# Optimization experiments

Measured on AMD Instinct MI355X. Metric: run time of the kernel, lower is better.

The kernel has to match this reference:

```python
import jax, jax.numpy as jnp
import numpy as np

N_ROUTINGS = 3
NEG_SLOPE = 0.01  # torch leaky_relu default


def l2norm(x, eps=1e-12):
    # torch.nn.functional.normalize along dim=1
    n = jnp.sqrt(jnp.sum(x * x, axis=1, keepdims=True))
    return x / jnp.maximum(n, eps)


def seg_softmax(w, seg, n):
    # numerically-stable softmax over edges grouped by node id `seg`
    m = jax.ops.segment_max(w, seg, num_segments=n)
    e = jnp.exp(w - m[seg])
    s = jax.ops.segment_sum(e, seg, num_segments=n)
    return e / (s[seg] + 1e-16)


def setup_inputs() -> dict:
    key = jax.random.key(0)
    ks = jax.random.split(key, 8)
    NU, NI, D, F, E, B = 100000, 50000, 64, 2048, 2000000, 4096
    return {
        "Gum": jax.random.normal(ks[0], (NU, D), dtype=jnp.float32),
        "feat": jax.random.normal(ks[1], (NI, F), dtype=jnp.float32),
        "proj_w": jax.random.normal(ks[2], (F, D), dtype=jnp.float32) * 0.02,
        "proj_b": jax.random.normal(ks[3], (D,), dtype=jnp.float32) * 0.02,
        "rows": jax.random.randint(ks[4], (E,), 0, NU, dtype=jnp.int32),
        "cols": jax.random.randint(ks[5], (E,), 0, NI, dtype=jnp.int32),
        "user": jax.random.randint(ks[6], (B,), 0, NU, dtype=jnp.int32),
        "pos": jax.random.randint(ks[7], (B,), 0, NI, dtype=jnp.int32),
    }


def reference(Gum, feat, proj_w, proj_b, rows, cols, user, pos):
    NU = Gum.shape[0]
    NI = feat.shape[0]
    # user multimodal preference embeddings, normalized
    gum = l2norm(Gum)
    # item multimodal content: normalize features, project, leaky_relu, normalize
    gim = l2norm(jax.nn.leaky_relu(l2norm(feat) @ proj_w + proj_b, NEG_SLOPE))
    cols_attr = gim[cols]  # [E, D] gathered once (as in original)
    # routing iterations: refine user preference via attention over item neighbors
    for _ in range(N_ROUTINGS):
        rows_attr = gum[rows]                                   # [E, D] gather
        w = jax.nn.leaky_relu(jnp.sum(rows_attr * cols_attr, -1), NEG_SLOPE)
        alpha = seg_softmax(w, rows, NU)                        # per-user softmax
        upd = jax.ops.segment_sum(alpha[:, None] * cols_attr, rows, num_segments=NU)
        gum = l2norm(gum + upd)
    # final refining layer on the full (symmetric) interaction graph
    rows_attr = gum[rows]
    w = jax.nn.leaky_relu(jnp.sum(rows_attr * cols_attr, -1), NEG_SLOPE)
    a_u = seg_softmax(w, rows, NU)
    a_i = seg_softmax(w, cols, NI)
    hat_u = jax.ops.segment_sum(a_u[:, None] * cols_attr, rows, num_segments=NU)
    hat_i = jax.ops.segment_sum(a_i[:, None] * rows_attr, cols, num_segments=NI)
    gu = gum + hat_u   # all_x_m += all_x_hat_m (user part)
    gi = gim + hat_i   # (item part)
    # model.forward: elementwise dot of gathered user/item embeddings
    xui = jnp.sum(gu[user] * gi[pos], axis=1)  # [B]
    return xui
```

## Files before the change

kernel.cpp:

```cpp
#include <hip/hip_runtime.h>
#include <math.h>

#define RCAP 16

__device__ __forceinline__ int wsumi(int v) {
#pragma unroll
    for (int o = 32; o > 0; o >>= 1) v += __shfl_xor(v, o, 64);
    return v;
}
__device__ __forceinline__ float grp16_sum(float v) {
    v += __shfl_xor(v, 1, 64);
    v += __shfl_xor(v, 2, 64);
    v += __shfl_xor(v, 4, 64);
    v += __shfl_xor(v, 8, 64);
    return v;
}
__device__ __forceinline__ float xgrp_sum(float v) {
    v += __shfl_xor(v, 16, 64);
    v += __shfl_xor(v, 32, 64);
    return v;
}
__device__ __forceinline__ float4 xgrp_sum4(float4 a) {
    a.x = xgrp_sum(a.x); a.y = xgrp_sum(a.y);
    a.z = xgrp_sum(a.z); a.w = xgrp_sum(a.w);
    return a;
}

__global__ void k_gim(const float* __restrict__ feat, const float* __restrict__ W,
                      const float* __restrict__ bias, float* __restrict__ gim,
                      int NI, int F) {
    __shared__ float As[64][17];
    __shared__ float Bs[16][64];
    __shared__ float rn[64];
    const int tid = threadIdx.x;
    const int r0 = blockIdx.x * 64;
    const int tr = tid >> 4, tc = tid & 15;
    const int lrow = tid >> 2, lk = (tid & 3) * 4;
    float acc[4][4];
#pragma unroll
    for (int i = 0; i < 4; ++i)
#pragma unroll
        for (int j = 0; j < 4; ++j) acc[i][j] = 0.f;
    float ssq = 0.f;
    const bool rowok = (r0 + lrow) < NI;

    for (int kb = 0; kb < F; kb += 16) {
        float4 av = make_float4(0.f, 0.f, 0.f, 0.f);
        if (rowok) av = *(const float4*)(feat + (size_t)(r0 + lrow) * F + kb + lk);
        As[lrow][lk + 0] = av.x; As[lrow][lk + 1] = av.y;
        As[lrow][lk + 2] = av.z; As[lrow][lk + 3] = av.w;
        ssq += av.x * av.x + av.y * av.y + av.z * av.z + av.w * av.w;
        float4 bv = *(const float4*)(W + (size_t)(kb + (tid >> 4)) * 64 + (tid & 15) * 4);
        *(float4*)&Bs[tid >> 4][(tid & 15) * 4] = bv;
        __syncthreads();
#pragma unroll
        for (int kk = 0; kk < 16; ++kk) {
            float a[4], b[4];
#pragma unroll
            for (int i = 0; i < 4; ++i) a[i] = As[tr * 4 + i][kk];
#pragma unroll
            for (int j = 0; j < 4; ++j) b[j] = Bs[kk][tc * 4 + j];
#pragma unroll
            for (int i = 0; i < 4; ++i)
#pragma unroll
                for (int j = 0; j < 4; ++j) acc[i][j] += a[i] * b[j];
        }
        __syncthreads();
    }
    ssq += __shfl_xor(ssq, 1, 64);
    ssq += __shfl_xor(ssq, 2, 64);
    if ((tid & 3) == 0) rn[lrow] = ssq;
    __syncthreads();

    float bc[4];
#pragma unroll
    for (int j = 0; j < 4; ++j) bc[j] = bias[tc * 4 + j];
#pragma unroll
    for (int i = 0; i < 4; ++i) {
        int r = tr * 4 + i;
        float inv = 1.0f / fmaxf(sqrtf(rn[r]), 1e-12f);
        float v[4], rs = 0.f;
#pragma unroll
        for (int j = 0; j < 4; ++j) {
            float x = acc[i][j] * inv + bc[j];
            x = x > 0.f ? x : 0.01f * x;
            v[j] = x; rs += x * x;
        }
        rs += __shfl_xor(rs, 1, 64); rs += __shfl_xor(rs, 2, 64);
        rs += __shfl_xor(rs, 4, 64); rs += __shfl_xor(rs, 8, 64);
        float sc = 1.0f / fmaxf(sqrtf(rs), 1e-12f);
        int gr = r0 + r;
        if (gr < NI) {
            float4 o = make_float4(v[0] * sc, v[1] * sc, v[2] * sc, v[3] * sc);
            *(float4*)(gim + (size_t)gr * 64 + tc * 4) = o;
        }
    }
}

__global__ void k_hist(const int* __restrict__ rows, const int* __restrict__ cols, int E,
                       int* __restrict__ cu, int* __restrict__ ci,
                       int* __restrict__ ranku, int* __restrict__ ranki) {
    for (int e = blockIdx.x * blockDim.x + threadIdx.x; e < E; e += gridDim.x * blockDim.x) {
        ranku[e] = atomicAdd(&cu[rows[e]], 1);
        ranki[e] = atomicAdd(&ci[cols[e]], 1);
    }
}

__global__ void k_bsum(const int* __restrict__ cnt, int n, int* __restrict__ bsum) {
    int i = blockIdx.x * 256 + threadIdx.x;
    int v = (i < n) ? cnt[i] : 0;
    v = wsumi(v);
    __shared__ int sm[4];
    if ((threadIdx.x & 63) == 0) sm[threadIdx.x >> 6] = v;
    __syncthreads();
    if (threadIdx.x == 0) bsum[blockIdx.x] = sm[0] + sm[1] + sm[2] + sm[3];
}

__global__ void k_bscan(const int* __restrict__ bsum, int nb, int* __restrict__ bscan) {
    __shared__ int sd[512];
    int tid = threadIdx.x;
    int v = (tid < nb) ? bsum[tid] : 0;
    sd[tid] = v;
    __syncthreads();
    for (int off = 1; off < 512; off <<= 1) {
        int t = (tid >= off) ? sd[tid - off] : 0;
        __syncthreads();
        sd[tid] += t;
        __syncthreads();
    }
    if (tid < nb) bscan[tid] = sd[tid] - v;
}

__global__ void k_scan2(const int* __restrict__ cnt, int n, const int* __restrict__ bscan,
                        int* __restrict__ ptr) {
    __shared__ int sd[256];
    int tid = threadIdx.x;
    int i = blockIdx.x * 256 + tid;
    int v = (i < n) ? cnt[i] : 0;
    sd[tid] = v;
    __syncthreads();
    for (int off = 1; off < 256; off <<= 1) {
        int t = (tid >= off) ? sd[tid - off] : 0;
        __syncthreads();
        sd[tid] += t;
        __syncthreads();
    }
    if (i < n) ptr[i + 1] = sd[tid] + bscan[blockIdx.x];
    if (blockIdx.x == 0 && tid == 0) ptr[0] = 0;
}

__global__ void k_scatter(const int* __restrict__ rows, const int* __restrict__ cols, int E,
                          const int* __restrict__ ranku, const int* __restrict__ ranki,
                          const int* __restrict__ rptr, const int* __restrict__ cptr,
                          int2* __restrict__ csr, int* __restrict__ csc_r) {
    for (int e = blockIdx.x * blockDim.x + threadIdx.x; e < E; e += gridDim.x * blockDim.x) {
        int r = rows[e], c = cols[e];
        int pu = rptr[r] + ranku[e];
        int pi = cptr[c] + ranki[e];
        csr[pu] = make_int2(c, pi);
        csc_r[pi] = r;
    }
}

__global__ void __launch_bounds__(256) k_route(
        const float* __restrict__ Gum, const float* __restrict__ gim,
        const int* __restrict__ rptr, const int2* __restrict__ csr,
        float* __restrict__ gum_out, float* __restrict__ gu,
        float* __restrict__ expw_csc, int NU) {
    __shared__ float tile[4 * RCAP * 64];
    int wid = (blockIdx.x * blockDim.x + threadIdx.x) >> 6;
    int lane = threadIdx.x & 63;
    if (wid >= NU) return;
    const int q = lane >> 4, r = lane & 15;
    float* my = tile + (threadIdx.x >> 6) * (RCAP * 64);
    const size_t ubase = (size_t)wid * 64 + 4 * r;

    float4 gl = *(const float4*)(Gum + ubase);
    float s2 = grp16_sum(gl.x * gl.x + gl.y * gl.y + gl.z * gl.z + gl.w * gl.w);
    float inv = 1.0f / fmaxf(sqrtf(s2), 1e-12f);
    gl.x *= inv; gl.y *= inv; gl.z *= inv; gl.w *= inv;

    const int st = rptr[wid], en = rptr[wid + 1];
    const int enc = min(en, st + RCAP);

    {
        float s = 0.f;
        float4 acc = make_float4(0.f, 0.f, 0.f, 0.f);
        for (int j0 = st; j0 < en; j0 += 4) {
            int j = j0 + q;
            bool valid = j < en;
            int c = valid ? csr[j].x : 0;
            float4 gv = *(const float4*)(gim + (size_t)c * 64 + 4 * r);
            if (j < enc) *(float4*)(my + (j - st) * 64 + 4 * r) = gv;
            float d = grp16_sum(gl.x * gv.x + gl.y * gv.y + gl.z * gv.z + gl.w * gv.w);
            float w = d > 0.f ? d : 0.01f * d;
            float ew = valid ? __expf(w) : 0.f;
            s += ew;
            acc.x += ew * gv.x; acc.y += ew * gv.y;
            acc.z += ew * gv.z; acc.w += ew * gv.w;
        }
        s = xgrp_sum(s);
        acc = xgrp_sum4(acc);
        float invs = 1.0f / (s + 1e-16f);
        gl.x += acc.x * invs; gl.y += acc.y * invs;
        gl.z += acc.z * invs; gl.w += acc.w * invs;
        s2 = grp16_sum(gl.x * gl.x + gl.y * gl.y + gl.z * gl.z + gl.w * gl.w);
        inv = 1.0f / fmaxf(sqrtf(s2), 1e-12f);
        gl.x *= inv; gl.y *= inv; gl.z *= inv; gl.w *= inv;
    }

    for (int it = 0; it < 2; ++it) {
        float s = 0.f;
        float4 acc = make_float4(0.f, 0.f, 0.f, 0.f);
        for (int j0 = st; j0 < en; j0 += 4) {
            int j = j0 + q;
            bool valid = j < en;
            float4 gv;
            if (j < enc) {
                gv = *(const float4*)(my + (j - st) * 64 + 4 * r);
            } else {
                int c = valid ? csr[j].x : 0;
                gv = *(const float4*)(gim + (size_t)c * 64 + 4 * r);
            }
            float d = grp16_sum(gl.x * gv.x + gl.y * gv.y + gl.z * gv.z + gl.w * gv.w);
            float w = d > 0.f ? d : 0.01f * d;
            float ew = valid ? __expf(w) : 0.f;
            s += ew;
            acc.x += ew * gv.x; acc.y += ew * gv.y;
            acc.z += ew * gv.z; acc.w += ew * gv.w;
        }
        s = xgrp_sum(s);
        acc = xgrp_sum4(acc);
        float invs = 1.0f / (s + 1e-16f);
        gl.x += acc.x * invs; gl.y += acc.y * invs;
        gl.z += acc.z * invs; gl.w += acc.w * invs;
        s2 = grp16_sum(gl.x * gl.x + gl.y * gl.y + gl.z * gl.z + gl.w * gl.w);
        inv = 1.0f / fmaxf(sqrtf(s2), 1e-12f);
        gl.x *= inv; gl.y *= inv; gl.z *= inv; gl.w *= inv;
    }
    if (q == 0) *(float4*)(gum_out + ubase) = gl;

    float s = 0.f;
    float4 acc = make_float4(0.f, 0.f, 0.f, 0.f);
    for (int j0 = st; j0 < en; j0 += 4) {
        int j = j0 + q;
        bool valid = j < en;
        float4 gv;
        if (j < enc) {
            gv = *(const float4*)(my + (j - st) * 64 + 4 * r);
        } else {
            int c = valid ? csr[j].x : 0;
            gv = *(const float4*)(gim + (size_t)c * 64 + 4 * r);
        }
        float d = grp16_sum(gl.x * gv.x + gl.y * gv.y + gl.z * gv.z + gl.w * gv.w);
        float w = d > 0.f ? d : 0.01f * d;
        float ew = valid ? __expf(w) : 0.f;
        if (valid && r == 0) expw_csc[csr[j].y] = ew;
        s += ew;
        acc.x += ew * gv.x; acc.y += ew * gv.y;
        acc.z += ew * gv.z; acc.w += ew * gv.w;
    }
    s = xgrp_sum(s);
    acc = xgrp_sum4(acc);
    float invs = 1.0f / (s + 1e-16f);
    if (q == 0) {
        float4 o = make_float4(gl.x + acc.x * invs, gl.y + acc.y * invs,
                               gl.z + acc.z * invs, gl.w + acc.w * invs);
        *(float4*)(gu + ubase) = o;
    }
}

__global__ void k_item(const float* __restrict__ gum, const float* __restrict__ gim,
                       const int* __restrict__ cptr, const int* __restrict__ csc_r,
                       const float* __restrict__ expw_csc,
                       float* __restrict__ gi, int NI) {
    int wid = (blockIdx.x * blockDim.x + threadIdx.x) >> 6;
    int lane = threadIdx.x & 63;
    if (wid >= NI) return;
    const int q = lane >> 4, r = lane & 15;
    const int st = cptr[wid], en = cptr[wid + 1];
    float s = 0.f;
    float4 acc = make_float4(0.f, 0.f, 0.f, 0.f);
    for (int j0 = st; j0 < en; j0 += 4) {
        int j = j0 + q;
        bool valid = j < en;
        int rr = valid ? csc_r[j] : 0;
        float ew = valid ? expw_csc[j] : 0.f;
        float4 gv = *(const float4*)(gum + (size_t)rr * 64 + 4 * r);
        s += ew;
        acc.x += ew * gv.x; acc.y += ew * gv.y;
        acc.z += ew * gv.z; acc.w += ew * gv.w;
    }
    s = xgrp_sum(s);
    acc = xgrp_sum4(acc);
    float invs = 1.0f / (s + 1e-16f);
    if (q == 0) {
        const size_t ib = (size_t)wid * 64 + 4 * r;
        float4 gm = *(const float4*)(gim + ib);
        float4 o = make_float4(gm.x + acc.x * invs, gm.y + acc.y * invs,
                               gm.z + acc.z * invs, gm.w + acc.w * invs);
        *(float4*)(gi + ib) = o;
    }
}

__global__ void k_out(const float* __restrict__ gu, const float* __restrict__ gi,
                      const int* __restrict__ user, const int* __restrict__ pos,
                      float* __restrict__ out, int B) {
    int wid = (blockIdx.x * blockDim.x + threadIdx.x) >> 6;
    int lane = threadIdx.x & 63;
    if (wid >= B) return;
    float v = gu[(size_t)user[wid] * 64 + lane] * gi[(size_t)pos[wid] * 64 + lane];
#pragma unroll
    for (int o = 32; o > 0; o >>= 1) v += __shfl_xor(v, o, 64);
    if (lane == 0) out[wid] = v;
}

extern "C" void kernel_launch(void* const* d_in, const int* in_sizes, int n_in,
                              void* d_out, int out_size, void* d_ws, size_t ws_size,
                              hipStream_t stream) {
    const float* Gum  = (const float*)d_in[0];
    const float* feat = (const float*)d_in[1];
    const float* W    = (const float*)d_in[2];
    const float* bias = (const float*)d_in[3];
    const int* rows   = (const int*)d_in[4];
    const int* cols   = (const int*)d_in[5];
    const int* user   = (const int*)d_in[6];
    const int* pos    = (const int*)d_in[7];
    float* out = (float*)d_out;

    const int D  = in_sizes[3];
    const int NU = in_sizes[0] / D;
    const int F  = in_sizes[2] / D;
    const int NI = in_sizes[1] / F;
    const int E  = in_sizes[4];
    const int B  = in_sizes[6];

    char* p = (char*)d_ws;
    auto alloc = [&](size_t bytes) -> void* {
        void* r = (void*)p;
        p += (bytes + 255) / 256 * 256;
        return r;
    };
    float* gum     = (float*)alloc((size_t)NU * 64 * 4);
    float* gim     = (float*)alloc((size_t)NI * 64 * 4);
    float* gu      = (float*)alloc((size_t)NU * 64 * 4);
    float* gi      = (float*)alloc((size_t)NI * 64 * 4);
    float* expw    = (float*)alloc((size_t)E * 4);
    int* rptr      = (int*)alloc((size_t)(NU + 1) * 4);
    int* cptr      = (int*)alloc((size_t)(NI + 1) * 4);
    int* cu        = (int*)alloc((size_t)NU * 4);
    int* ci        = (int*)alloc((size_t)NI * 4);
    int* ranku     = (int*)alloc((size_t)E * 4);
    int* ranki     = (int*)alloc((size_t)E * 4);
    int2* csr      = (int2*)alloc((size_t)E * 8);
    int* csc_r     = (int*)alloc((size_t)E * 4);
    int* bsumU     = (int*)alloc(1024 * 4);
    int* bscanU    = (int*)alloc(1024 * 4);
    int* bsumI     = (int*)alloc(1024 * 4);
    int* bscanI    = (int*)alloc(1024 * 4);

    const int gU = (NU + 255) / 256;
    const int gI = (NI + 255) / 256;

    hipMemsetAsync(cu, 0, (size_t)NU * 4, stream);
    hipMemsetAsync(ci, 0, (size_t)NI * 4, stream);
    k_hist<<<2048, 256, 0, stream>>>(rows, cols, E, cu, ci, ranku, ranki);

    k_bsum<<<gU, 256, 0, stream>>>(cu, NU, bsumU);
    k_bscan<<<1, 512, 0, stream>>>(bsumU, gU, bscanU);
    k_scan2<<<gU, 256, 0, stream>>>(cu, NU, bscanU, rptr);

    k_bsum<<<gI, 256, 0, stream>>>(ci, NI, bsumI);
    k_bscan<<<1, 512, 0, stream>>>(bsumI, gI, bscanI);
    k_scan2<<<gI, 256, 0, stream>>>(ci, NI, bscanI, cptr);

    k_scatter<<<2048, 256, 0, stream>>>(rows, cols, E, ranku, ranki, rptr, cptr, csr, csc_r);

    k_gim<<<(NI + 63) / 64, 256, 0, stream>>>(feat, W, bias, gim, NI, F);
    k_route<<<(NU + 3) / 4, 256, 0, stream>>>(Gum, gim, rptr, csr, gum, gu, expw, NU);
    k_item<<<(NI + 3) / 4, 256, 0, stream>>>(gum, gim, cptr, csc_r, expw, gi, NI);
    k_out<<<(B + 3) / 4, 256, 0, stream>>>(gu, gi, user, pos, out, B);
}
```

Measured before the change: 1.285 ms.

## Retile projection GEMM to 32-row blocks with transposed A tile and K=32

The feature-projection GEMM kernel now uses 32-row blocks with a 32-deep K step. The A tile is stored transposed so each thread reads its two rows with one float2 and its columns with one float4. Global loads for the next step are issued before the barrier, which drops one sync per iteration. Doubling the block count gives more parallelism and shorter latency chains on this memory-bound 400MB feature read. The cost is a 2x4 per-thread tile with less register reuse of B, so W is re-read more often.

```diff
diff --git a/kernel.cpp b/kernel.cpp
--- a/kernel.cpp
+++ b/kernel.cpp
@@ -26,58 +26,56 @@
     return a;
 }
 
-__global__ void k_gim(const float* __restrict__ feat, const float* __restrict__ W,
-                      const float* __restrict__ bias, float* __restrict__ gim,
-                      int NI, int F) {
-    __shared__ float As[64][17];
-    __shared__ float Bs[16][64];
-    __shared__ float rn[64];
+__global__ void __launch_bounds__(256) k_gim(
+        const float* __restrict__ feat, const float* __restrict__ W,
+        const float* __restrict__ bias, float* __restrict__ gim,
+        int NI, int F) {
+    __shared__ float As[32][34];
+    __shared__ float Bs[32][64];
+    __shared__ float rn[32];
     const int tid = threadIdx.x;
-    const int r0 = blockIdx.x * 64;
+    const int r0 = blockIdx.x * 32;
+    const int lrow = tid >> 3, lk4 = (tid & 7) * 4;
     const int tr = tid >> 4, tc = tid & 15;
-    const int lrow = tid >> 2, lk = (tid & 3) * 4;
-    float acc[4][4];
-#pragma unroll
-    for (int i = 0; i < 4; ++i)
-#pragma unroll
-        for (int j = 0; j < 4; ++j) acc[i][j] = 0.f;
+    float acc[2][4] = {{0.f,0.f,0.f,0.f},{0.f,0.f,0.f,0.f}};
     float ssq = 0.f;
     const bool rowok = (r0 + lrow) < NI;
-
-    for (int kb = 0; kb < F; kb += 16) {
+    const float* featp = feat + (size_t)(r0 + lrow) * F + lk4;
+
+    for (int kb = 0; kb < F; kb += 32) {
         float4 av = make_float4(0.f, 0.f, 0.f, 0.f);
-        if (rowok) av = *(const float4*)(feat + (size_t)(r0 + lrow) * F + kb + lk);
-        As[lrow][lk + 0] = av.x; As[lrow][lk + 1] = av.y;
-        As[lrow][lk + 2] = av.z; As[lrow][lk + 3] = av.w;
+        if (rowok) av = *(const float4*)(featp + kb);
+        float4 bv0 = *(const float4*)(W + (size_t)(kb + tr) * 64 + tc * 4);
+        float4 bv1 = *(const float4*)(W + (size_t)(kb + 16 + tr) * 64 + tc * 4);
+        __syncthreads();
+        As[lk4 + 0][lrow] = av.x; As[lk4 + 1][lrow] = av.y;
+        As[lk4 + 2][lrow] = av.z; As[lk4 + 3][lrow] = av.w;
         ssq += av.x * av.x + av.y * av.y + av.z * av.z + av.w * av.w;
-        float4 bv = *(const float4*)(W + (size_t)(kb + (tid >> 4)) * 64 + (tid & 15) * 4);
-        *(float4*)&Bs[tid >> 4][(tid & 15) * 4] = bv;
-        __syncthreads();
-#pragma unroll
-        for (int kk = 0; kk < 16; ++kk) {
-            float a[4], b[4];
-#pragma unroll
-            for (int i = 0; i < 4; ++i) a[i] = As[tr * 4 + i][kk];
-#pragma unroll
-            for (int j = 0; j < 4; ++j) b[j] = Bs[kk][tc * 4 + j];
-#pragma unroll
-            for (int i = 0; i < 4; ++i)
-#pragma unroll
-                for (int j = 0; j < 4; ++j) acc[i][j] += a[i] * b[j];
-        }
-        __syncthreads();
+        *(float4*)&Bs[tr][tc * 4] = bv0;
+        *(float4*)&Bs[16 + tr][tc * 4] = bv1;
+        __syncthreads();
+#pragma unroll
+        for (int kk = 0; kk < 32; ++kk) {
+            float2 a = *(const float2*)&As[kk][tr * 2];
+            float4 b = *(const float4*)&Bs[kk][tc * 4];
+            acc[0][0] += a.x * b.x; acc[0][1] += a.x * b.y;
+            acc[0][2] += a.x * b.z; acc[0][3] += a.x * b.w;
+            acc[1][0] += a.y * b.x; acc[1][1] += a.y * b.y;
+            acc[1][2] += a.y * b.z; acc[1][3] += a.y * b.w;
+        }
     }
     ssq += __shfl_xor(ssq, 1, 64);
     ssq += __shfl_xor(ssq, 2, 64);
-    if ((tid & 3) == 0) rn[lrow] = ssq;
+    ssq += __shfl_xor(ssq, 4, 64);
+    if ((tid & 7) == 0) rn[lrow] = ssq;
     __syncthreads();
 
     float bc[4];
 #pragma unroll
     for (int j = 0; j < 4; ++j) bc[j] = bias[tc * 4 + j];
 #pragma unroll
-    for (int i = 0; i < 4; ++i) {
-        int r = tr * 4 + i;
+    for (int i = 0; i < 2; ++i) {
+        int r = tr * 2 + i;
         float inv = 1.0f / fmaxf(sqrtf(rn[r]), 1e-12f);
         float v[4], rs = 0.f;
 #pragma unroll
@@ -376,7 +374,7 @@
 
     k_scatter<<<2048, 256, 0, stream>>>(rows, cols, E, ranku, ranki, rptr, cptr, csr, csc_r);
 
-    k_gim<<<(NI + 63) / 64, 256, 0, stream>>>(feat, W, bias, gim, NI, F);
+    k_gim<<<(NI + 31) / 32, 256, 0, stream>>>(feat, W, bias, gim, NI, F);
     k_route<<<(NU + 3) / 4, 256, 0, stream>>>(Gum, gim, rptr, csr, gum, gu, expw, NU);
     k_item<<<(NI + 3) / 4, 256, 0, stream>>>(gum, gim, cptr, csc_r, expw, gi, NI);
     k_out<<<(B + 3) / 4, 256, 0, stream>>>(gu, gi, user, pos, out, B);
```

Result: no change. 1.284 ms (-0.1%).
